# Performance work log

Measured on AMD Instinct MI355X. Metric: run time of the kernel, lower is better.

The kernel has to match this reference:

```python
import jax, jax.numpy as jnp
import numpy as np

N_NODES = 100000
N_EDGES = 1600000
F_IN = 128
F_HID = 128
N_CLASSES = 40
PERIODS = 1


def gcn_conv(x, edge_index, edge_weight, W, b):
    """PyG GCNConv: add self-loops (weight 1), symmetric normalization, scatter-add aggregation."""
    N = x.shape[0]
    row, col = edge_index[0], edge_index[1]
    loop = jnp.arange(N)
    row_f = jnp.concatenate([row, loop])
    col_f = jnp.concatenate([col, loop])
    w_f = jnp.concatenate([edge_weight, jnp.ones((N,), dtype=x.dtype)])
    deg = jax.ops.segment_sum(w_f, col_f, num_segments=N)
    dinv = jnp.where(deg > 0, jax.lax.rsqrt(deg), jnp.zeros_like(deg))
    norm = dinv[row_f] * w_f * dinv[col_f]            # [E+N]
    xw = x @ W                                        # [N, F_out]
    msg = norm[:, None] * xw[row_f]                   # [E+N, F_out] gather
    out = jax.ops.segment_sum(msg, col_f, num_segments=N)  # scatter-add
    return out + b


def setup_inputs() -> dict:
    key = jax.random.key(0)
    ks = jax.random.split(key, 8)
    x = jax.random.normal(ks[0], (N_NODES, F_IN), dtype=jnp.float32)
    edge_index = jax.random.randint(ks[1], (2, N_EDGES), 0, N_NODES, dtype=jnp.int64)
    edge_weight = jax.random.uniform(ks[2], (N_EDGES,), dtype=jnp.float32)
    attention = jax.random.uniform(ks[3], (PERIODS,), dtype=jnp.float32)
    W1 = jax.random.normal(ks[4], (F_IN, F_HID), dtype=jnp.float32) * (1.0 / np.sqrt(F_IN))
    b1 = jnp.zeros((F_HID,), dtype=jnp.float32)
    W2 = jax.random.normal(ks[5], (F_HID, N_CLASSES), dtype=jnp.float32) * (1.0 / np.sqrt(F_HID))
    b2 = jnp.zeros((N_CLASSES,), dtype=jnp.float32)
    return {"x": x, "edge_index": edge_index, "edge_weight": edge_weight,
            "attention": attention, "W1": W1, "b1": b1, "W2": W2, "b2": b2}


def reference(x, edge_index, edge_weight, attention, W1, b1, W2, b2):
    periods = attention.shape[0]
    h0 = x.reshape(x.shape[0], x.shape[1], 1)          # matches x.view(N, F, 1)
    probs = jax.nn.softmax(attention, axis=0)
    H_accum = 0.0
    for period in range(periods):                      # periods == 1 structurally
        H_accum = H_accum + probs[period] * gcn_conv(h0[:, :, period], edge_index, edge_weight, W1, b1)
    h = jax.nn.relu(H_accum)
    h = gcn_conv(h, edge_index, edge_weight, W2, b2)
    return jax.nn.softmax(h, axis=1)
```

## Files before the change

kernel.cpp:

```cpp
#include <hip/hip_runtime.h>
#include <hip/hip_bf16.h>
#include <hip/hip_fp16.h>

#define N_NODES 100000
#define N_EDGES 1600000


__global__ void init_kernel(unsigned long long* packed) {
    int i = blockIdx.x * 256 + threadIdx.x;
    if (i < N_NODES) packed[i] = 0ULL;
}

__global__ void count_kernel(const int* __restrict__ ei, const float* __restrict__ w,
                             unsigned long long* packed, int* __restrict__ seq) {
    int e = blockIdx.x * 256 + threadIdx.x;
    if (e < N_EDGES) {
        int c = ei[N_EDGES + e];
        unsigned int fw = (unsigned int)rintf(w[e] * 1048576.0f);
        unsigned long long old = atomicAdd(&packed[c], (1ULL << 32) | (unsigned long long)fw);
        seq[e] = (int)(old >> 32);
    }
}

__global__ void scanA_kernel(const unsigned long long* __restrict__ packed,
                             int* __restrict__ off, int* __restrict__ bsum,
                             float* __restrict__ dinv) {
    __shared__ int s[1024];
    int t = threadIdx.x;
    int i = blockIdx.x * 1024 + t;
    unsigned long long pk = (i < N_NODES) ? packed[i] : 0ULL;
    int v = (int)(pk >> 32);
    if (i < N_NODES) {
        float deg = 1.0f + (float)(unsigned int)(pk & 0xffffffffULL) * (1.0f / 1048576.0f);
        dinv[i] = rsqrtf(deg);
    }
    s[t] = v; __syncthreads();
    #pragma unroll
    for (int d = 1; d < 1024; d <<= 1) {
        int x = (t >= d) ? s[t - d] : 0;
        __syncthreads();
        s[t] += x;
        __syncthreads();
    }
    if (i < N_NODES) off[i] = s[t] - v;
    if (t == 1023) bsum[blockIdx.x] = s[1023];
}

__global__ void scanB_kernel(int* bsum, int nb) {
    __shared__ int s[1024];
    int t = threadIdx.x;
    int v = (t < nb) ? bsum[t] : 0;
    s[t] = v; __syncthreads();
    #pragma unroll
    for (int d = 1; d < 1024; d <<= 1) {
        int x = (t >= d) ? s[t - d] : 0;
        __syncthreads();
        s[t] += x;
        __syncthreads();
    }
    if (t < nb) bsum[t] = s[t] - v;
}

__global__ void scanC_kernel(int* __restrict__ off, const int* __restrict__ bsum) {
    int i = blockIdx.x * 1024 + threadIdx.x;
    if (i < N_NODES) off[i] += bsum[blockIdx.x];
    if (i == 0) off[N_NODES] = N_EDGES;
}

__global__ void fill_kernel(const int* __restrict__ ei, const float* __restrict__ w,
                            const float* __restrict__ dinv, const int* __restrict__ off,
                            const int* __restrict__ seq, int2* __restrict__ epack) {
    int e = blockIdx.x * 256 + threadIdx.x;
    if (e < N_EDGES) {
        int r = ei[e];
        int c = ei[N_EDGES + e];
        int p = off[c] + seq[e];
        float nrm = dinv[r] * w[e] * dinv[c];
        epack[p] = make_int2(r, __float_as_int(nrm));
    }
}


__global__ __launch_bounds__(256) void gemm1_kernel(const float* __restrict__ X,
                                                    const float* __restrict__ W,
                                                    __half* __restrict__ XW) {
    __shared__ float sA[32][132];
    __shared__ float sB[32][132];
    int t = threadIdx.x;
    int row0 = blockIdx.x * 128;
    int tc = t & 15, tr = t >> 4;
    int m0 = tr * 8, n0 = tc * 8;
    float acc[8][8] = {};
    for (int kt = 0; kt < 128; kt += 32) {
        #pragma unroll
        for (int q = 0; q < 4; ++q) {
            int g = t + q * 256;
            int row = g >> 3;
            int c4 = g & 7;
            float4 v = make_float4(0.f, 0.f, 0.f, 0.f);
            int grow = row0 + row;
            if (grow < N_NODES) v = *(const float4*)(X + (size_t)grow * 128 + kt + c4 * 4);
            sA[c4 * 4 + 0][row] = v.x;
            sA[c4 * 4 + 1][row] = v.y;
            sA[c4 * 4 + 2][row] = v.z;
            sA[c4 * 4 + 3][row] = v.w;
        }
        #pragma unroll
        for (int q = 0; q < 4; ++q) {
            int g = t + q * 256;
            int k = g >> 5, n4 = g & 31;
            *(float4*)(&sB[k][n4 * 4]) = *(const float4*)(W + (kt + k) * 128 + n4 * 4);
        }
        __syncthreads();
        #pragma unroll
        for (int k = 0; k < 32; ++k) {
            float4 a0 = *(const float4*)(&sA[k][m0]);
            float4 a1 = *(const float4*)(&sA[k][m0 + 4]);
            float4 b0 = *(const float4*)(&sB[k][n0]);
            float4 b1v = *(const float4*)(&sB[k][n0 + 4]);
            float a[8] = {a0.x, a0.y, a0.z, a0.w, a1.x, a1.y, a1.z, a1.w};
            float b[8] = {b0.x, b0.y, b0.z, b0.w, b1v.x, b1v.y, b1v.z, b1v.w};
            #pragma unroll
            for (int j = 0; j < 8; ++j)
                #pragma unroll
                for (int i = 0; i < 8; ++i) acc[j][i] += a[j] * b[i];
        }
        __syncthreads();
    }
    #pragma unroll
    for (int j = 0; j < 8; ++j) {
        int grow = row0 + m0 + j;
        if (grow < N_NODES) {
            __align__(16) __half2 hp[4];
            hp[0] = __floats2half2_rn(acc[j][0], acc[j][1]);
            hp[1] = __floats2half2_rn(acc[j][2], acc[j][3]);
            hp[2] = __floats2half2_rn(acc[j][4], acc[j][5]);
            hp[3] = __floats2half2_rn(acc[j][6], acc[j][7]);
            *(float4*)(XW + (size_t)grow * 128 + n0) = *(const float4*)hp;
        }
    }
}


__global__ __launch_bounds__(256) void agg1f_kernel(const __half* __restrict__ XW,
                                                    const int* __restrict__ off,
                                                    const int2* __restrict__ epack,
                                                    const float* __restrict__ dinv,
                                                    const float* __restrict__ b1,
                                                    const float* __restrict__ W2,
                                                    __half* __restrict__ HW) {
    __shared__ __align__(16) float sW2[5120];
    __shared__ __align__(16) float sH[4][128];
    int t = threadIdx.x;
    #pragma unroll
    for (int q = 0; q < 5; ++q) {
        int g = t + q * 256;
        ((float4*)sW2)[g] = ((const float4*)W2)[g];
    }

    int wv = __builtin_amdgcn_readfirstlane(t) >> 6;
    int n = blockIdx.x * 4 + wv;
    int l = t & 63;
    const __half2* XW2 = (const __half2*)XW;
    float di = dinv[n];
    float self = di * di;
    float2 v = __half22float2(XW2[(size_t)n * 64 + l]);
    float accx[8], accy[8];
    accx[0] = self * v.x; accy[0] = self * v.y;
    #pragma unroll
    for (int k = 1; k < 8; ++k) { accx[k] = 0.f; accy[k] = 0.f; }
    int e0 = off[n], e1 = off[n + 1];
    int emain = e0 + ((e1 - e0) & ~7);
    for (int base = e0; base < emain; base += 8) {
        int2 p[8];
        #pragma unroll
        for (int k = 0; k < 8; ++k) p[k] = epack[base + k];
        #pragma unroll
        for (int k = 0; k < 8; ++k) {
            float2 g = __half22float2(XW2[(size_t)p[k].x * 64 + l]);
            float w = __int_as_float(p[k].y);
            accx[k] += w * g.x;
            accy[k] += w * g.y;
        }
    }
    for (int e = emain; e < e1; ++e) {
        int2 p = epack[e];
        float2 g = __half22float2(XW2[(size_t)p.x * 64 + l]);
        float w = __int_as_float(p.y);
        accx[0] += w * g.x;
        accy[0] += w * g.y;
    }
    float ax = ((accx[0] + accx[1]) + (accx[2] + accx[3])) + ((accx[4] + accx[5]) + (accx[6] + accx[7]));
    float ay = ((accy[0] + accy[1]) + (accy[2] + accy[3])) + ((accy[4] + accy[5]) + (accy[6] + accy[7]));
    float2 bb = ((const float2*)b1)[l];
    float hx = fmaxf(ax + bb.x, 0.f);
    float hy = fmaxf(ay + bb.y, 0.f);
    ((float2*)sH[wv])[l] = make_float2(hx, hy);
    __syncthreads();

    if (l < 40) {
        const float* hrow = sH[wv];
        float dot = 0.f;
        #pragma unroll 4
        for (int k = 0; k < 128; k += 4) {
            float4 h4 = *(const float4*)(hrow + k);
            dot += h4.x * sW2[(k + 0) * 40 + l];
            dot += h4.y * sW2[(k + 1) * 40 + l];
            dot += h4.z * sW2[(k + 2) * 40 + l];
            dot += h4.w * sW2[(k + 3) * 40 + l];
        }
        HW[(size_t)n * 40 + l] = __float2half_rn(dot);
    }
}


__global__ __launch_bounds__(256) void agg2_kernel(const __half* __restrict__ HW,
                                                   const int* __restrict__ off,
                                                   const int2* __restrict__ epack,
                                                   const float* __restrict__ dinv,
                                                   const float* __restrict__ b2,
                                                   float* __restrict__ out) {
    int t = threadIdx.x;
    int wv = __builtin_amdgcn_readfirstlane(t) >> 6;
    int n = blockIdx.x * 4 + wv;
    int l = t & 63;
    if (n >= N_NODES) return;
    bool act = (l < 40);
    int ll = act ? l : l - 40;
    float di = dinv[n];
    float acc[8];
    acc[0] = di * di * __half2float(HW[(size_t)n * 40 + ll]);
    #pragma unroll
    for (int k = 1; k < 8; ++k) acc[k] = 0.f;
    int e0 = off[n], e1 = off[n + 1];
    int emain = e0 + ((e1 - e0) & ~7);
    for (int base = e0; base < emain; base += 8) {
        int2 p[8];
        #pragma unroll
        for (int k = 0; k < 8; ++k) p[k] = epack[base + k];
        #pragma unroll
        for (int k = 0; k < 8; ++k) {
            float g = __half2float(HW[(size_t)p[k].x * 40 + ll]);
            acc[k] += __int_as_float(p[k].y) * g;
        }
    }
    for (int e = emain; e < e1; ++e) {
        int2 p = epack[e];
        acc[0] += __int_as_float(p.y) * __half2float(HW[(size_t)p.x * 40 + ll]);
    }
    float a = ((acc[0] + acc[1]) + (acc[2] + acc[3])) + ((acc[4] + acc[5]) + (acc[6] + acc[7]));
    a += b2[ll];
    float m = act ? a : -1e30f;
    #pragma unroll
    for (int d = 32; d; d >>= 1) m = fmaxf(m, __shfl_xor(m, d, 64));
    float pexp = act ? expf(a - m) : 0.f;
    float s = pexp;
    #pragma unroll
    for (int d = 32; d; d >>= 1) s += __shfl_xor(s, d, 64);
    if (act) out[(size_t)n * 40 + l] = pexp / s;
}


extern "C" void kernel_launch(void* const* d_in, const int* in_sizes, int n_in,
                              void* d_out, int out_size, void* d_ws, size_t ws_size,
                              hipStream_t stream) {
    const float* x  = (const float*)d_in[0];
    const int*   ei = (const int*)d_in[1];
    const float* ew = (const float*)d_in[2];
    const float* W1 = (const float*)d_in[4];
    const float* b1 = (const float*)d_in[5];
    const float* W2 = (const float*)d_in[6];
    const float* b2 = (const float*)d_in[7];
    float* out = (float*)d_out;

    char* p = (char*)d_ws;
    auto alloc = [&](size_t bytes) -> void* {
        void* r = (void*)p;
        p += (bytes + 511) & ~(size_t)511;
        return r;
    };
    unsigned long long* packed = (unsigned long long*)alloc((size_t)N_NODES * 8);
    float* dinv   = (float*)alloc((size_t)N_NODES * 4);
    int*   off    = (int*)alloc((size_t)(N_NODES + 1) * 4);
    int*   bsum   = (int*)alloc(1024 * 4);
    int*   seq    = (int*)alloc((size_t)N_EDGES * 4);
    int2*  epack  = (int2*)alloc((size_t)N_EDGES * 8);
    __half* XW    = (__half*)alloc((size_t)N_NODES * 128 * 2);
    __half* HW    = (__half*)alloc((size_t)N_NODES * 40 * 2);

    int nblk_n = (N_NODES + 255) / 256;
    int nblk_e = (N_EDGES + 255) / 256;
    int nblk_s = (N_NODES + 1023) / 1024;

    hipLaunchKernelGGL(init_kernel,  dim3(nblk_n), dim3(256), 0, stream, packed);
    hipLaunchKernelGGL(count_kernel, dim3(nblk_e), dim3(256), 0, stream, ei, ew, packed, seq);
    hipLaunchKernelGGL(scanA_kernel, dim3(nblk_s), dim3(1024), 0, stream, packed, off, bsum, dinv);
    hipLaunchKernelGGL(scanB_kernel, dim3(1), dim3(1024), 0, stream, bsum, nblk_s);
    hipLaunchKernelGGL(scanC_kernel, dim3(nblk_s), dim3(1024), 0, stream, off, bsum);
    hipLaunchKernelGGL(fill_kernel,  dim3(nblk_e), dim3(256), 0, stream, ei, ew, dinv, off, seq, epack);

    hipLaunchKernelGGL(gemm1_kernel, dim3((N_NODES + 127) / 128), dim3(256), 0, stream, x, W1, XW);
    hipLaunchKernelGGL(agg1f_kernel, dim3(N_NODES / 4), dim3(256), 0, stream,
                       XW, off, epack, dinv, b1, W2, HW);
    hipLaunchKernelGGL(agg2_kernel,  dim3((N_NODES + 3) / 4), dim3(256), 0, stream,
                       HW, off, epack, dinv, b2, out);
}
```

Before: 337.9 us.

## Fuse edge counting into GEMM1 launch and store W2 as half in LDS

The edge-count atomic pass and the first dense GEMM now run in one launch: the first block range does the XW GEMM and the remaining blocks do the per-edge atomic counting. This lets the compute-bound GEMM overlap with the atomic-bound counting and removes one launch. Separately, agg1f stages W2 in shared memory as fp16 instead of fp32, halving its LDS footprint, which may raise occupancy at the cost of a small precision loss in the second-layer weights.

```diff
diff --git a/kernel.cpp b/kernel.cpp
--- a/kernel.cpp
+++ b/kernel.cpp
@@ -4,6 +4,7 @@
 
 #define N_NODES 100000
 #define N_EDGES 1600000
+#define G1_BLOCKS 782
 
 
 __global__ void init_kernel(unsigned long long* packed) {
@@ -11,82 +12,27 @@
     if (i < N_NODES) packed[i] = 0ULL;
 }
 
-__global__ void count_kernel(const int* __restrict__ ei, const float* __restrict__ w,
-                             unsigned long long* packed, int* __restrict__ seq) {
-    int e = blockIdx.x * 256 + threadIdx.x;
-    if (e < N_EDGES) {
-        int c = ei[N_EDGES + e];
-        unsigned int fw = (unsigned int)rintf(w[e] * 1048576.0f);
-        unsigned long long old = atomicAdd(&packed[c], (1ULL << 32) | (unsigned long long)fw);
-        seq[e] = (int)(old >> 32);
-    }
-}
-
-__global__ void scanA_kernel(const unsigned long long* __restrict__ packed,
-                             int* __restrict__ off, int* __restrict__ bsum,
-                             float* __restrict__ dinv) {
-    __shared__ int s[1024];
-    int t = threadIdx.x;
-    int i = blockIdx.x * 1024 + t;
-    unsigned long long pk = (i < N_NODES) ? packed[i] : 0ULL;
-    int v = (int)(pk >> 32);
-    if (i < N_NODES) {
-        float deg = 1.0f + (float)(unsigned int)(pk & 0xffffffffULL) * (1.0f / 1048576.0f);
-        dinv[i] = rsqrtf(deg);
-    }
-    s[t] = v; __syncthreads();
-    #pragma unroll
-    for (int d = 1; d < 1024; d <<= 1) {
-        int x = (t >= d) ? s[t - d] : 0;
-        __syncthreads();
-        s[t] += x;
-        __syncthreads();
-    }
-    if (i < N_NODES) off[i] = s[t] - v;
-    if (t == 1023) bsum[blockIdx.x] = s[1023];
-}
-
-__global__ void scanB_kernel(int* bsum, int nb) {
-    __shared__ int s[1024];
-    int t = threadIdx.x;
-    int v = (t < nb) ? bsum[t] : 0;
-    s[t] = v; __syncthreads();
-    #pragma unroll
-    for (int d = 1; d < 1024; d <<= 1) {
-        int x = (t >= d) ? s[t - d] : 0;
-        __syncthreads();
-        s[t] += x;
-        __syncthreads();
-    }
-    if (t < nb) bsum[t] = s[t] - v;
-}
-
-__global__ void scanC_kernel(int* __restrict__ off, const int* __restrict__ bsum) {
-    int i = blockIdx.x * 1024 + threadIdx.x;
-    if (i < N_NODES) off[i] += bsum[blockIdx.x];
-    if (i == 0) off[N_NODES] = N_EDGES;
-}
-
-__global__ void fill_kernel(const int* __restrict__ ei, const float* __restrict__ w,
-                            const float* __restrict__ dinv, const int* __restrict__ off,
-                            const int* __restrict__ seq, int2* __restrict__ epack) {
-    int e = blockIdx.x * 256 + threadIdx.x;
-    if (e < N_EDGES) {
-        int r = ei[e];
-        int c = ei[N_EDGES + e];
-        int p = off[c] + seq[e];
-        float nrm = dinv[r] * w[e] * dinv[c];
-        epack[p] = make_int2(r, __float_as_int(nrm));
-    }
-}
-
-
-__global__ __launch_bounds__(256) void gemm1_kernel(const float* __restrict__ X,
-                                                    const float* __restrict__ W,
-                                                    __half* __restrict__ XW) {
+
+__global__ __launch_bounds__(256) void k1_kernel(const float* __restrict__ X,
+                                                 const float* __restrict__ W,
+                                                 __half* __restrict__ XW,
+                                                 const int* __restrict__ ei,
+                                                 const float* __restrict__ ew,
+                                                 unsigned long long* packed,
+                                                 int* __restrict__ seq) {
     __shared__ float sA[32][132];
     __shared__ float sB[32][132];
     int t = threadIdx.x;
+    if (blockIdx.x >= G1_BLOCKS) {
+        int e = (blockIdx.x - G1_BLOCKS) * 256 + t;
+        if (e < N_EDGES) {
+            int c = ei[N_EDGES + e];
+            unsigned int fw = (unsigned int)rintf(ew[e] * 1048576.0f);
+            unsigned long long old = atomicAdd(&packed[c], (1ULL << 32) | (unsigned long long)fw);
+            seq[e] = (int)(old >> 32);
+        }
+        return;
+    }
     int row0 = blockIdx.x * 128;
     int tc = t & 15, tr = t >> 4;
     int m0 = tr * 8, n0 = tc * 8;
@@ -141,6 +87,64 @@
     }
 }
 
+__global__ void scanA_kernel(const unsigned long long* __restrict__ packed,
+                             int* __restrict__ off, int* __restrict__ bsum,
+                             float* __restrict__ dinv) {
+    __shared__ int s[1024];
+    int t = threadIdx.x;
+    int i = blockIdx.x * 1024 + t;
+    unsigned long long pk = (i < N_NODES) ? packed[i] : 0ULL;
+    int v = (int)(pk >> 32);
+    if (i < N_NODES) {
+        float deg = 1.0f + (float)(unsigned int)(pk & 0xffffffffULL) * (1.0f / 1048576.0f);
+        dinv[i] = rsqrtf(deg);
+    }
+    s[t] = v; __syncthreads();
+    #pragma unroll
+    for (int d = 1; d < 1024; d <<= 1) {
+        int x = (t >= d) ? s[t - d] : 0;
+        __syncthreads();
+        s[t] += x;
+        __syncthreads();
+    }
+    if (i < N_NODES) off[i] = s[t] - v;
+    if (t == 1023) bsum[blockIdx.x] = s[1023];
+}
+
+__global__ void scanB_kernel(int* bsum, int nb) {
+    __shared__ int s[1024];
+    int t = threadIdx.x;
+    int v = (t < nb) ? bsum[t] : 0;
+    s[t] = v; __syncthreads();
+    #pragma unroll
+    for (int d = 1; d < 1024; d <<= 1) {
+        int x = (t >= d) ? s[t - d] : 0;
+        __syncthreads();
+        s[t] += x;
+        __syncthreads();
+    }
+    if (t < nb) bsum[t] = s[t] - v;
+}
+
+__global__ void scanC_kernel(int* __restrict__ off, const int* __restrict__ bsum) {
+    int i = blockIdx.x * 1024 + threadIdx.x;
+    if (i < N_NODES) off[i] += bsum[blockIdx.x];
+    if (i == 0) off[N_NODES] = N_EDGES;
+}
+
+__global__ void fill_kernel(const int* __restrict__ ei, const float* __restrict__ w,
+                            const float* __restrict__ dinv, const int* __restrict__ off,
+                            const int* __restrict__ seq, int2* __restrict__ epack) {
+    int e = blockIdx.x * 256 + threadIdx.x;
+    if (e < N_EDGES) {
+        int r = ei[e];
+        int c = ei[N_EDGES + e];
+        int p = off[c] + seq[e];
+        float nrm = dinv[r] * w[e] * dinv[c];
+        epack[p] = make_int2(r, __float_as_int(nrm));
+    }
+}
+
 
 __global__ __launch_bounds__(256) void agg1f_kernel(const __half* __restrict__ XW,
                                                     const int* __restrict__ off,
@@ -149,13 +153,15 @@
                                                     const float* __restrict__ b1,
                                                     const float* __restrict__ W2,
                                                     __half* __restrict__ HW) {
-    __shared__ __align__(16) float sW2[5120];
+    __shared__ __align__(16) __half sW2h[5120];
     __shared__ __align__(16) float sH[4][128];
     int t = threadIdx.x;
-    #pragma unroll
-    for (int q = 0; q < 5; ++q) {
+    const float2* W22 = (const float2*)W2;
+    #pragma unroll
+    for (int q = 0; q < 10; ++q) {
         int g = t + q * 256;
-        ((float4*)sW2)[g] = ((const float4*)W2)[g];
+        float2 v = W22[g];
+        ((__half2*)sW2h)[g] = __floats2half2_rn(v.x, v.y);
     }
 
     int wv = __builtin_amdgcn_readfirstlane(t) >> 6;
@@ -204,10 +210,10 @@
         #pragma unroll 4
         for (int k = 0; k < 128; k += 4) {
             float4 h4 = *(const float4*)(hrow + k);
-            dot += h4.x * sW2[(k + 0) * 40 + l];
-            dot += h4.y * sW2[(k + 1) * 40 + l];
-            dot += h4.z * sW2[(k + 2) * 40 + l];
-            dot += h4.w * sW2[(k + 3) * 40 + l];
+            dot += h4.x * __half2float(sW2h[(k + 0) * 40 + l]);
+            dot += h4.y * __half2float(sW2h[(k + 1) * 40 + l]);
+            dot += h4.z * __half2float(sW2h[(k + 2) * 40 + l]);
+            dot += h4.w * __half2float(sW2h[(k + 3) * 40 + l]);
         }
         HW[(size_t)n * 40 + l] = __float2half_rn(dot);
     }
@@ -293,13 +299,13 @@
     int nblk_s = (N_NODES + 1023) / 1024;
 
     hipLaunchKernelGGL(init_kernel,  dim3(nblk_n), dim3(256), 0, stream, packed);
-    hipLaunchKernelGGL(count_kernel, dim3(nblk_e), dim3(256), 0, stream, ei, ew, packed, seq);
+    hipLaunchKernelGGL(k1_kernel,    dim3(G1_BLOCKS + nblk_e), dim3(256), 0, stream,
+                       x, W1, XW, ei, ew, packed, seq);
     hipLaunchKernelGGL(scanA_kernel, dim3(nblk_s), dim3(1024), 0, stream, packed, off, bsum, dinv);
     hipLaunchKernelGGL(scanB_kernel, dim3(1), dim3(1024), 0, stream, bsum, nblk_s);
     hipLaunchKernelGGL(scanC_kernel, dim3(nblk_s), dim3(1024), 0, stream, off, bsum);
     hipLaunchKernelGGL(fill_kernel,  dim3(nblk_e), dim3(256), 0, stream, ei, ew, dinv, off, seq, epack);
 
-    hipLaunchKernelGGL(gemm1_kernel, dim3((N_NODES + 127) / 128), dim3(256), 0, stream, x, W1, XW);
     hipLaunchKernelGGL(agg1f_kernel, dim3(N_NODES / 4), dim3(256), 0, stream,
                        XW, off, epack, dinv, b1, W2, HW);
     hipLaunchKernelGGL(agg2_kernel,  dim3((N_NODES + 3) / 4), dim3(256), 0, stream,
```

Measured after the change: 310.3 us. 1.09x faster.
